# Kernel optimization log

Measured on AMD Instinct MI355X. Metric: run time of the kernel, lower is better.

The kernel has to match this reference:

```python
import jax, jax.numpy as jnp
import numpy as np

B, S, D = 4, 2048, 768
H = 12
DH = D // H  # 64
DF = 2048
THETA = 10000.0
EPS = 1e-5


def setup_inputs() -> dict:
    key = jax.random.key(0)
    ks = jax.random.split(key, 8)
    sc = 0.02  # keep activations numerically tame
    return {
        "x": jax.random.normal(ks[0], (B, S, D), jnp.float32),
        "ln1_w": jnp.ones((D,), jnp.float32),
        "ln2_w": jnp.ones((D,), jnp.float32),
        "p_q": jax.random.normal(ks[1], (D, D), jnp.float32) * sc,
        "p_k": jax.random.normal(ks[2], (D, D), jnp.float32) * sc,
        "p_v": jax.random.normal(ks[3], (D, D), jnp.float32) * sc,
        "p_o": jax.random.normal(ks[4], (D, D), jnp.float32) * sc,
        "w1": jax.random.normal(ks[5], (DF, D), jnp.float32) * sc,
        "w2": jax.random.normal(ks[6], (D, DF), jnp.float32) * sc,
        "w3": jax.random.normal(ks[7], (DF, D), jnp.float32) * sc,
    }


def _rmsnorm(x, w):
    # matches torch: fp32 compute, mean-square + eps
    rms = jnp.sqrt(jnp.mean(x * x, axis=-1, keepdims=True) + EPS)
    return x / rms * w


def _rope(t):
    # t: [B, H, S, DH]; rotation per RoPE matrix: pairs (2k, 2k+1)
    pos = jnp.arange(S, dtype=jnp.float32)[:, None]            # [S,1]
    k = jnp.arange(DH // 2, dtype=jnp.float32)[None, :]        # [1,DH/2]
    ang = pos / (THETA ** (2.0 * k / DH))                      # [S,DH/2]
    cos, sin = jnp.cos(ang), jnp.sin(ang)
    t2 = t.reshape(*t.shape[:-1], DH // 2, 2)
    x0, x1 = t2[..., 0], t2[..., 1]
    o0 = cos * x0 - sin * x1
    o1 = sin * x0 + cos * x1
    return jnp.stack([o0, o1], axis=-1).reshape(t.shape)


def reference(x, ln1_w, ln2_w, p_q, p_k, p_v, p_o, w1, w2, w3):
    # --- attention sublayer ---
    h = _rmsnorm(x, ln1_w)                                     # [B,S,D]
    Wq = p_q.reshape(H, DH, D)
    Wk = p_k.reshape(H, DH, D)
    Wv = p_v.reshape(H, DH, D)
    q = _rope(jnp.einsum('bsd,hed->bhse', h, Wq))              # [B,H,S,DH]
    k = _rope(jnp.einsum('bsd,hed->bhse', h, Wk))
    v = jnp.einsum('bsd,hed->bhse', h, Wv)
    scores = jnp.einsum('bhqe,bhke->bhqk', q, k)               # [B,H,S,S]
    mask = jnp.tril(jnp.ones((S, S), bool))
    scores = jnp.where(mask, scores, -jnp.inf)
    attn = jax.nn.softmax(scores / jnp.sqrt(jnp.float32(DH)), axis=-1)
    ctx = jnp.einsum('bhqk,bhke->bhqe', attn, v)               # [B,H,S,DH]
    ctx = jnp.transpose(ctx, (0, 2, 1, 3)).reshape(B, S, D)    # [B,S,D]
    x = x + ctx @ p_o.T
    # --- SwiGLU FFN sublayer ---
    h2 = _rmsnorm(x, ln2_w)
    u1 = h2 @ w1.T
    u1 = u1 * jax.nn.sigmoid(u1)                               # SiLU
    u3 = h2 @ w3.T
    x = x + (u1 * u3) @ w2.T
    return x
```

## Files before the change

### kernel.cpp

```cpp
#include <hip/hip_runtime.h>
#include <stdint.h>

#define B_  4
#define S_  2048
#define D_  768
#define H_  12
#define DH_ 64
#define DF_ 2048
#define M_  (B_*S_)
#define NQKV 2304
#define N13  4096

typedef __attribute__((ext_vector_type(8))) short bf16x8;
typedef __attribute__((ext_vector_type(4))) short bf16x4;
typedef __attribute__((ext_vector_type(4))) float f32x4;
typedef unsigned short u16;

#if !defined(__HIP_DEVICE_COMPILE__)
  #define MFMA_K16(A,B,C) (C)
#elif __has_builtin(__builtin_amdgcn_mfma_f32_16x16x16_bf16)
  #define MFMA_K16(A,B,C) __builtin_amdgcn_mfma_f32_16x16x16_bf16((A),(B),(C),0,0,0)
#else
  #define MFMA_K16(A,B,C) __builtin_amdgcn_mfma_f32_16x16x16bf16_1k((A),(B),(C),0,0,0)
#endif

__device__ __forceinline__ float bf2f(u16 v) {
  union { uint32_t u; float f; } x; x.u = ((uint32_t)v) << 16; return x.f;
}
__device__ __forceinline__ u16 f2bf(float f) {
  union { float f; uint32_t u; } x; x.f = f;
  uint32_t r = x.u + 0x7FFFu + ((x.u >> 16) & 1u);
  return (u16)(r >> 16);
}
__device__ __forceinline__ void gl_lds16(const u16* g, u16* l) {
  __builtin_amdgcn_global_load_lds((const __attribute__((address_space(1))) uint32_t*)g,
                                   (__attribute__((address_space(3))) uint32_t*)l, 16, 0, 0);
}

__global__ __launch_bounds__(256) void cast_all_kernel(const float* __restrict__ pq,
                                                       const float* __restrict__ pk,
                                                       const float* __restrict__ pv,
                                                       const float* __restrict__ po,
                                                       const float* __restrict__ w2,
                                                       u16* __restrict__ wqkv,
                                                       u16* __restrict__ wob,
                                                       u16* __restrict__ w2b) {
  int bidx = blockIdx.x;
  const float* src; u16* dst; int off;
  if (bidx < 576)       { src = pq; dst = wqkv;           off = bidx; }
  else if (bidx < 1152) { src = pk; dst = wqkv + 589824;  off = bidx - 576; }
  else if (bidx < 1728) { src = pv; dst = wqkv + 1179648; off = bidx - 1152; }
  else if (bidx < 2304) { src = po; dst = wob;            off = bidx - 1728; }
  else                  { src = w2; dst = w2b;            off = bidx - 2304; }
  int i = off * 256 + threadIdx.x;
  float4 v = ((const float4*)src)[i];
  ushort4 o;
  o.x = f2bf(v.x); o.y = f2bf(v.y); o.z = f2bf(v.z); o.w = f2bf(v.w);
  ((ushort4*)dst)[i] = o;
}

__global__ __launch_bounds__(192) void cast_w13_kernel(const float* __restrict__ w1,
                                                       const float* __restrict__ w3,
                                                       u16* __restrict__ out) {
  int j = blockIdx.x, which = blockIdx.y;
  const float* src = (which ? w3 : w1) + (size_t)j * D_;
  int fr = (j >> 4) * 32 + (j & 15) + which * 16;
  u16* dst = out + (size_t)fr * D_;
  int t = threadIdx.x;
  float4 v = ((const float4*)src)[t];
  ushort4 o;
  o.x = f2bf(v.x); o.y = f2bf(v.y); o.z = f2bf(v.z); o.w = f2bf(v.w);
  ((ushort4*)dst)[t] = o;
}

__global__ __launch_bounds__(256) void rmsnorm_kernel(const float* __restrict__ x,
                                                      const float* __restrict__ w,
                                                      u16* __restrict__ out) {
  int row = blockIdx.x, tid = threadIdx.x;
  const float* xr = x + (size_t)row * D_;
  float v0 = xr[tid], v1 = xr[tid + 256], v2 = xr[tid + 512];
  float ss = v0 * v0 + v1 * v1 + v2 * v2;
  #pragma unroll
  for (int m = 32; m >= 1; m >>= 1) ss += __shfl_xor(ss, m, 64);
  __shared__ float red[4];
  if ((tid & 63) == 0) red[tid >> 6] = ss;
  __syncthreads();
  float tot = red[0] + red[1] + red[2] + red[3];
  float r = rsqrtf(tot * (1.0f / D_) + 1e-5f);
  u16* o = out + (size_t)row * D_;
  o[tid]       = f2bf(v0 * r * w[tid]);
  o[tid + 256] = f2bf(v1 * r * w[tid + 256]);
  o[tid + 512] = f2bf(v2 * r * w[tid + 512]);
}

template<int MT, int EPI>
__global__ __launch_bounds__(256) void gemm_bt_kernel(const u16* __restrict__ A,
                                                      const u16* __restrict__ W,
                                                      void* __restrict__ Cout,
                                                      const float* __restrict__ res,
                                                      u16* __restrict__ vTout,
                                                      int K, int N) {
  constexpr int ABELEMS = MT * 64 + 128 * 64;
  constexpr int SMELEMS = (EPI == 3 && 128 * 132 > ABELEMS) ? 128 * 132 : ABELEMS;
  __shared__ __align__(16) u16 smem[SMELEMS];
  u16* As = smem;
  u16* Bs = smem + MT * 64;
  constexpr int MI = MT / 32;
  int tid = threadIdx.x;
  int wave = tid >> 6, lane = tid & 63;
  int quad = lane >> 4, l16 = lane & 15;
  int wr = (wave >> 1) * (MT / 2), wc = (wave & 1) * 64;
  int gx = gridDim.x;
  int lin = blockIdx.y * gx + blockIdx.x;
  int cpx = (gx * gridDim.y) >> 3;
  int nlin = (lin & 7) * cpx + (lin >> 3);
  int m0 = (nlin / gx) * MT, n0 = (nlin % gx) * 128;
  f32x4 acc[MI][4] = {};
  for (int kt = 0; kt < K; kt += 64) {
    __syncthreads();
    #pragma unroll
    for (int i = 0; i < MT / 32; ++i) {
      int idx = i * 256 + tid;
      int r = idx >> 3, c = idx & 7;
      gl_lds16(&A[(size_t)(m0 + r) * K + kt + ((c ^ (r & 7)) * 8)], &As[(i * 256 + wave * 64) * 8]);
    }
    #pragma unroll
    for (int i = 0; i < 4; ++i) {
      int idx = i * 256 + tid;
      int r = idx >> 3, c = idx & 7;
      gl_lds16(&W[(size_t)(n0 + r) * K + kt + ((c ^ (r & 7)) * 8)], &Bs[(i * 256 + wave * 64) * 8]);
    }
    __syncthreads();
    #pragma unroll
    for (int ks = 0; ks < 2; ++ks) {
      bf16x8 af[MI], bf[4];
      int sw = ((ks * 4 + quad) ^ (l16 & 7)) * 8;
      #pragma unroll
      for (int t = 0; t < MI; ++t)
        af[t] = *(const bf16x8*)&As[(wr + t * 16 + l16) * 64 + sw];
      #pragma unroll
      for (int t = 0; t < 4; ++t)
        bf[t] = *(const bf16x8*)&Bs[(wc + t * 16 + l16) * 64 + sw];
      #pragma unroll
      for (int mt = 0; mt < MI; ++mt)
        #pragma unroll
        for (int nt = 0; nt < 4; ++nt)
          acc[mt][nt] = __builtin_amdgcn_mfma_f32_16x16x32_bf16(af[mt], bf[nt], acc[mt][nt], 0, 0, 0);
    }
  }

  if (EPI == 3 && n0 >= 1536) {
    __syncthreads();
    #pragma unroll
    for (int mt = 0; mt < MI; ++mt) {
      int sloc = wr + mt * 16 + quad * 4;
      #pragma unroll
      for (int nt = 0; nt < 4; ++nt) {
        int col = wc + nt * 16 + l16;
        ushort4 o;
        o.x = f2bf(acc[mt][nt][0]); o.y = f2bf(acc[mt][nt][1]);
        o.z = f2bf(acc[mt][nt][2]); o.w = f2bf(acc[mt][nt][3]);
        *(ushort4*)&smem[col * 132 + sloc] = o;
      }
    }
    __syncthreads();
    int b = m0 >> 11, sblk = m0 & 2047;
    #pragma unroll
    for (int i = 0; i < 8; ++i) {
      int idx = i * 256 + tid;
      int row = idx >> 4, c16 = idx & 15;
      uint4 d = *(const uint4*)&smem[row * 132 + c16 * 8];
      int vg = n0 - 1536 + row;
      int h = vg >> 6, dh = vg & 63;
      *(uint4*)&vTout[((size_t)(b * H_ + h) * 64 + dh) * (size_t)S_ + sblk + c16 * 8] = d;
    }
  } else if (EPI == 3) {
    bool isq = (n0 < 768);
    float osc = isq ? 0.18033688f : 1.0f;
    #pragma unroll
    for (int mt = 0; mt < MI; ++mt) {
      int r0 = m0 + wr + mt * 16 + quad * 4;
      int pos0 = r0 & 2047;
      #pragma unroll
      for (int nt = 0; nt < 4; ++nt) {
        int col = n0 + wc + nt * 16 + l16;
        int kk = (col & 63) >> 1;
        float freq = exp2f(-0.41524101186092035f * (float)kk);
        bool odd = (col & 1);
        #pragma unroll
        for (int r = 0; r < 4; ++r) {
          float own = acc[mt][nt][r];
          float pv = __shfl_xor(own, 1, 64);
          float ang = (float)(pos0 + r) * freq;
          float sv, cv;
          __sincosf(ang, &sv, &cv);
          float o = odd ? (sv * pv + cv * own) : (cv * own - sv * pv);
          ((u16*)Cout)[(size_t)(r0 + r) * N + col] = f2bf(o * osc);
        }
      }
    }
  } else {
    #pragma unroll
    for (int mt = 0; mt < MI; ++mt) {
      #pragma unroll
      for (int r = 0; r < 4; ++r) {
        int gr = m0 + wr + mt * 16 + quad * 4 + r;
        if (EPI == 2) {
          #pragma unroll
          for (int np = 0; np < 2; ++np) {
            float u1v = acc[mt][np * 2][r], u3v = acc[mt][np * 2 + 1][r];
            float sg = 1.0f / (1.0f + __builtin_amdgcn_exp2f(-u1v * 1.44269504f));
            float g = u1v * sg * u3v;
            int gc = (n0 >> 1) + (wave & 1) * 32 + np * 16 + l16;
            ((u16*)Cout)[(size_t)gr * (N >> 1) + gc] = f2bf(g);
          }
        } else {
          #pragma unroll
          for (int nt = 0; nt < 4; ++nt) {
            int gc = n0 + wc + nt * 16 + l16;
            size_t off = (size_t)gr * N + gc;
            float vv = acc[mt][nt][r];
            if (EPI == 1) ((float*)Cout)[off] = vv + res[off];
            else          ((u16*)Cout)[off] = f2bf(vv);
          }
        }
      }
    }
  }
}

#define FENCE() asm volatile("" ::: "memory")
#define BAR() do { FENCE(); __builtin_amdgcn_s_barrier(); FENCE(); } while (0)
#define LGKM0() do { asm volatile("s_waitcnt lgkmcnt(0)" ::: "memory"); \
                     __builtin_amdgcn_sched_barrier(0); } while (0)

template<int MH, int NH>
__device__ __forceinline__ void quad_mfma(f32x4 (&acc)[2][4][2][2],
                                          const bf16x8 (&ra)[4][2],
                                          const bf16x8 (&rb)[2][2]) {
  #pragma unroll
  for (int ks = 0; ks < 2; ++ks)
    #pragma unroll
    for (int mt = 0; mt < 4; ++mt)
      #pragma unroll
      for (int nt = 0; nt < 2; ++nt)
        acc[MH][mt][NH][nt] =
          __builtin_amdgcn_mfma_f32_16x16x32_bf16(ra[mt][ks], rb[nt][ks], acc[MH][mt][NH][nt], 0, 0, 0);
}

__device__ __forceinline__ void ld_af(bf16x8 (&rr)[4][2], const u16* base,
                                      int wrow, int l16, int quad) {
  #pragma unroll
  for (int mt = 0; mt < 4; ++mt)
    #pragma unroll
    for (int ks = 0; ks < 2; ++ks)
      rr[mt][ks] = *(const bf16x8*)&base[(wrow + mt * 16 + l16) * 64 +
                                         (((ks * 4 + quad) ^ (l16 & 7)) * 8)];
}
__device__ __forceinline__ void ld_bf(bf16x8 (&rr)[2][2], const u16* base,
                                      int wrow, int l16, int quad) {
  #pragma unroll
  for (int nt = 0; nt < 2; ++nt)
    #pragma unroll
    for (int ks = 0; ks < 2; ++ks)
      rr[nt][ks] = *(const bf16x8*)&base[(wrow + nt * 16 + l16) * 64 +
                                         (((ks * 4 + quad) ^ (l16 & 7)) * 8)];
}

template<int EPI, int K, int N>
__global__ __launch_bounds__(512, 2) void gemm256_kernel(const u16* __restrict__ A,
                                                         const u16* __restrict__ W,
                                                         void* __restrict__ Cout,
                                                         const float* __restrict__ res) {
  __shared__ __align__(16) u16 smem[2][2][2][128 * 64];
  int tid = threadIdx.x;
  int wave = tid >> 6, lane = tid & 63;
  int quad = lane >> 4, l16 = lane & 15;
  int wm = wave >> 2, wn = wave & 3;
  constexpr int GX = N / 256, NB = GX * (M_ / 256), CPX = NB / 8;
  int lin = blockIdx.y * GX + blockIdx.x;
  int nlin = (lin & 7) * CPX + (lin >> 3);
  int m0 = (nlin / GX) * 256, n0 = (nlin % GX) * 256;
  constexpr int NI = (K >> 6) >> 1;

  f32x4 acc[2][4][2][2] = {};
  bf16x8 rA[4][2], rBlo[2][2], rBhi[2][2];

  int r0 = tid >> 3, c0 = tid & 7;
  int scb = (c0 ^ (r0 & 7)) * 16;
  uint32_t offA = (uint32_t)(m0 + r0) * (uint32_t)(K * 2) + (uint32_t)scb;
  uint32_t offB = (uint32_t)(n0 + r0) * (uint32_t)(K * 2) + (uint32_t)scb;

  #define STG(kof, ab, h, bufi) do {                                               \
    const char* _s = (ab) ? (const char*)W : (const char*)A;                       \
    uint32_t _o = ((ab) ? offB : offA) + (uint32_t)((kof) + (h) * (128 * K * 2));  \
    u16* _d = &smem[bufi][ab][h][wave * 512];                                      \
    gl_lds16((const u16*)(_s + _o), _d);                                           \
    gl_lds16((const u16*)(_s + _o + 64 * K * 2), _d + 4096);                       \
  } while (0)

  int wrA = wm * 64, wrB = wn * 32;

  STG(0, 0, 0, 0); STG(0, 1, 0, 0); STG(0, 1, 1, 0); STG(0, 0, 1, 0);
  STG(128, 0, 0, 1); STG(128, 1, 0, 1); STG(128, 1, 1, 1); STG(128, 0, 1, 1);
  offA += 256; offB += 256;
  asm volatile("s_waitcnt vmcnt(8)" ::: "memory");
  BAR();
  ld_af(rA,   &smem[0][0][0][0], wrA, l16, quad);
  ld_bf(rBlo, &smem[0][1][0][0], wrB, l16, quad);
  LGKM0();
  BAR();

  #define G256_ITER(MORE) do {                                                     \
                                                                     \
    ld_bf(rBhi, &smem[0][1][1][0], wrB, l16, quad);                                \
    if (MORE) STG(0, 0, 0, 0);                                                     \
    BAR(); LGKM0();                                                                \
    __builtin_amdgcn_s_setprio(1); quad_mfma<0, 0>(acc, rA, rBlo);                 \
    __builtin_amdgcn_s_setprio(0); BAR();                                          \
                                                   \
    if (MORE) STG(0, 1, 0, 0);                                                     \
    BAR(); LGKM0();                                                                \
    __builtin_amdgcn_s_setprio(1); quad_mfma<0, 1>(acc, rA, rBhi);                 \
    __builtin_amdgcn_s_setprio(0);                                                 \
    ld_af(rA, &smem[0][0][1][0], wrA, l16, quad);                                  \
    BAR();                                                                         \
                                                   \
    if (MORE) STG(0, 1, 1, 0);                                                     \
    BAR(); LGKM0();                                                                \
    __builtin_amdgcn_s_setprio(1); quad_mfma<1, 0>(acc, rA, rBlo);                 \
    __builtin_amdgcn_s_setprio(0);                                                 \
    if (MORE) asm volatile("s_waitcnt vmcnt(6)" ::: "memory");                     \
    else      asm volatile("s_waitcnt vmcnt(0)" ::: "memory");                     \
    BAR();                                                                         \
                                    \
    ld_bf(rBlo, &smem[1][1][0][0], wrB, l16, quad);                                \
    if (MORE) STG(0, 0, 1, 0);                                                     \
    BAR(); LGKM0();                                                                \
    __builtin_amdgcn_s_setprio(1); quad_mfma<1, 1>(acc, rA, rBhi);                 \
    __builtin_amdgcn_s_setprio(0);                                                 \
    ld_af(rA, &smem[1][0][0][0], wrA, l16, quad);                                  \
    BAR();                                                                         \
                                                                \
    ld_bf(rBhi, &smem[1][1][1][0], wrB, l16, quad);                                \
    if (MORE) STG(128, 0, 0, 1);                                                   \
    BAR(); LGKM0();                                                                \
    __builtin_amdgcn_s_setprio(1); quad_mfma<0, 0>(acc, rA, rBlo);                 \
    __builtin_amdgcn_s_setprio(0); BAR();                                          \
                                                   \
    if (MORE) STG(128, 1, 0, 1);                                                   \
    BAR(); LGKM0();                                                                \
    __builtin_amdgcn_s_setprio(1); quad_mfma<0, 1>(acc, rA, rBhi);                 \
    __builtin_amdgcn_s_setprio(0);                                                 \
    ld_af(rA, &smem[1][0][1][0], wrA, l16, quad);                                  \
    BAR();                                                                         \
                                                   \
    if (MORE) STG(128, 1, 1, 1);                                                   \
    BAR(); LGKM0();                                                                \
    __builtin_amdgcn_s_setprio(1); quad_mfma<1, 0>(acc, rA, rBlo);                 \
    __builtin_amdgcn_s_setprio(0);                                                 \
    if (MORE) asm volatile("s_waitcnt vmcnt(6)" ::: "memory");                     \
    else      asm volatile("s_waitcnt vmcnt(0)" ::: "memory");                     \
    BAR();                                                                         \
                                    \
    if (MORE) ld_bf(rBlo, &smem[0][1][0][0], wrB, l16, quad);                      \
    if (MORE) STG(128, 0, 1, 1);                                                   \
    BAR(); LGKM0();                                                                \
    __builtin_amdgcn_s_setprio(1); quad_mfma<1, 1>(acc, rA, rBhi);                 \
    __builtin_amdgcn_s_setprio(0);                                                 \
    if (MORE) ld_af(rA, &smem[0][0][0][0], wrA, l16, quad);                        \
    BAR();                                                                         \
  } while (0)

  #pragma unroll 1
  for (int i = 0; i < NI - 1; ++i) {
    G256_ITER(true);
    offA += 256; offB += 256;
  }
  G256_ITER(false);
  #undef G256_ITER
  #undef STG

  if (EPI == 2) {
    const int Nh = N >> 1;
    #pragma unroll
    for (int mh = 0; mh < 2; ++mh)
      #pragma unroll
      for (int mt = 0; mt < 4; ++mt)
        #pragma unroll
        for (int r = 0; r < 4; ++r) {
          int gr = m0 + mh * 128 + wm * 64 + mt * 16 + quad * 4 + r;
          #pragma unroll
          for (int nh = 0; nh < 2; ++nh) {
            float u1v = acc[mh][mt][nh][0][r], u3v = acc[mh][mt][nh][1][r];
            float sg = 1.0f / (1.0f + __builtin_amdgcn_exp2f(-u1v * 1.44269504f));
            float g = u1v * sg * u3v;
            int gc = (n0 >> 1) + nh * 64 + wn * 16 + l16;
            ((u16*)Cout)[(size_t)gr * Nh + gc] = f2bf(g);
          }
        }
  } else if (EPI == 1) {
    #pragma unroll
    for (int mh = 0; mh < 2; ++mh)
      #pragma unroll
      for (int mt = 0; mt < 4; ++mt)
        #pragma unroll
        for (int r = 0; r < 4; ++r) {
          int gr = m0 + mh * 128 + wm * 64 + mt * 16 + quad * 4 + r;
          #pragma unroll
          for (int nh = 0; nh < 2; ++nh)
            #pragma unroll
            for (int nt = 0; nt < 2; ++nt) {
              int gc = n0 + nh * 128 + wn * 32 + nt * 16 + l16;
              size_t off = (size_t)gr * N + gc;
              ((float*)Cout)[off] = acc[mh][mt][nh][nt][r] + res[off];
            }
        }
  } else {
    #pragma unroll
    for (int mh = 0; mh < 2; ++mh)
      #pragma unroll
      for (int mt = 0; mt < 4; ++mt)
        #pragma unroll
        for (int r = 0; r < 4; ++r) {
          int gr = m0 + mh * 128 + wm * 64 + mt * 16 + quad * 4 + r;
          #pragma unroll
          for (int nh = 0; nh < 2; ++nh)
            #pragma unroll
            for (int nt = 0; nt < 2; ++nt) {
              int gc = n0 + nh * 128 + wn * 32 + nt * 16 + l16;
              ((u16*)Cout)[(size_t)gr * N + gc] = f2bf(acc[mh][mt][nh][nt][r]);
            }
        }
  }
}

__global__ __launch_bounds__(512, 4) void attn_kernel(const u16* __restrict__ qkv,
                                                      const u16* __restrict__ vT,
                                                      u16* __restrict__ ctx) {
  __shared__ __align__(16) u16 Ks[128 * 64];
  __shared__ __align__(16) u16 Vt[64 * 128];
  int bh = blockIdx.x;
  int qt = 15 - blockIdx.y;
  int b = bh / H_, h = bh % H_;
  const u16* qbase = qkv + (size_t)b * S_ * NQKV + h * DH_;
  const u16* kbase = qbase + 768;
  const u16* vtb   = vT + (size_t)bh * 64 * S_;
  int tid = threadIdx.x, wave = tid >> 6, lane = tid & 63;
  int quad = lane >> 4, l16 = lane & 15;
  const float MFIX = 12.0f;

  bf16x8 qf[2];
  int qrow = qt * 128 + wave * 16 + l16;
  qf[0] = *(const bf16x8*)&qbase[(size_t)qrow * NQKV + quad * 8];
  qf[1] = *(const bf16x8*)&qbase[(size_t)qrow * NQKV + 32 + quad * 8];
  f32x4 oacc[4] = {};
  float lsum = 0.f;
  int nkt = qt + 1;
  for (int kt = 0; kt < nkt; ++kt) {
    __syncthreads();
    #pragma unroll
    for (int i = 0; i < 2; ++i) {
      int idx = i * 512 + tid;
      int r = idx >> 3, c = idx & 7;
      gl_lds16(&kbase[(size_t)(kt * 128 + r) * NQKV + ((c ^ (r & 7)) * 8)],
               &Ks[(i * 512 + wave * 64) * 8]);
    }
    #pragma unroll
    for (int i = 0; i < 2; ++i) {
      int idx = i * 512 + tid;
      int d = idx >> 4, c16 = idx & 15;
      gl_lds16(&vtb[(size_t)d * S_ + kt * 128 + ((c16 ^ (d & 15)) * 8)],
               &Vt[(i * 512 + wave * 64) * 8]);
    }
    __syncthreads();
    bool diag = (kt == nkt - 1);
    #pragma unroll
    for (int t = 0; t < 8; ++t) {
      if (diag && t > wave) break;
      f32x4 sc = {};
      #pragma unroll
      for (int c = 0; c < 2; ++c) {
        bf16x8 kf = *(const bf16x8*)&Ks[(t * 16 + l16) * 64 + (((c * 4 + quad) ^ (l16 & 7)) * 8)];
        sc = __builtin_amdgcn_mfma_f32_16x16x32_bf16(kf, qf[c], sc, 0, 0, 0);
      }
      float p[4];
      #pragma unroll
      for (int r = 0; r < 4; ++r) p[r] = __builtin_amdgcn_exp2f(sc[r] - MFIX);
      if (diag && t == wave) {
        #pragma unroll
        for (int r = 0; r < 4; ++r)
          if (quad * 4 + r > l16) p[r] = 0.f;
      }
      lsum += (p[0] + p[1]) + (p[2] + p[3]);
      uint32_t lo = ((__float_as_uint(p[0]) + 0x8000u) >> 16) |
                    ((__float_as_uint(p[1]) + 0x8000u) & 0xFFFF0000u);
      uint32_t hi = ((__float_as_uint(p[2]) + 0x8000u) >> 16) |
                    ((__float_as_uint(p[3]) + 0x8000u) & 0xFFFF0000u);
      uint2 pk; pk.x = lo; pk.y = hi;
      bf16x4 pf = *(bf16x4*)&pk;
      #pragma unroll
      for (int n = 0; n < 4; ++n) {
        bf16x4 vf = *(const bf16x4*)&Vt[(n * 16 + l16) * 128 +
                                        (((t * 2 + (quad >> 1)) ^ l16) * 8) + (quad & 1) * 4];
        oacc[n] = MFMA_K16(vf, pf, oacc[n]);
      }
    }
  }
  float l = lsum;
  l += __shfl_xor(l, 16, 64);
  l += __shfl_xor(l, 32, 64);
  float inv = 1.0f / l;
  #pragma unroll
  for (int n = 0; n < 4; ++n) {
    ushort4 o;
    o.x = f2bf(oacc[n][0] * inv);
    o.y = f2bf(oacc[n][1] * inv);
    o.z = f2bf(oacc[n][2] * inv);
    o.w = f2bf(oacc[n][3] * inv);
    *(ushort4*)&ctx[(size_t)(b * S_ + qrow) * D_ + h * DH_ + n * 16 + quad * 4] = o;
  }
}

#define WQKV_OFF 0u
#define W13_OFF  3538944u
#define W2_OFF   9830400u
#define WO_OFF   12976128u
#define HB_OFF   14155776u
#define QKV_OFF  26738688u
#define VT_OFF   64487424u
#define X1_OFF   77070336u
#define G_OFF    102236160u

extern "C" void kernel_launch(void* const* d_in, const int* in_sizes, int n_in,
                              void* d_out, int out_size, void* d_ws, size_t ws_size,
                              hipStream_t stream) {
  const float* x    = (const float*)d_in[0];
  const float* ln1w = (const float*)d_in[1];
  const float* ln2w = (const float*)d_in[2];
  const float* pq   = (const float*)d_in[3];
  const float* pk   = (const float*)d_in[4];
  const float* pv   = (const float*)d_in[5];
  const float* po   = (const float*)d_in[6];
  const float* w1   = (const float*)d_in[7];
  const float* w2   = (const float*)d_in[8];
  const float* w3   = (const float*)d_in[9];
  char* ws = (char*)d_ws;
  u16* wqkv = (u16*)(ws + WQKV_OFF);
  u16* w13b = (u16*)(ws + W13_OFF);
  u16* w2b  = (u16*)(ws + W2_OFF);
  u16* wob  = (u16*)(ws + WO_OFF);
  u16* hb   = (u16*)(ws + HB_OFF);
  u16* qkvb = (u16*)(ws + QKV_OFF);
  u16* vtb  = (u16*)(ws + VT_OFF);
  u16* cb   = (u16*)(ws + HB_OFF);
  float* x1 = (float*)(ws + X1_OFF);
  u16* h2b  = (u16*)(ws + VT_OFF);
  u16* gb   = (u16*)(ws + G_OFF);

  cast_all_kernel<<<3840, 256, 0, stream>>>(pq, pk, pv, po, w2, wqkv, wob, w2b);
  cast_w13_kernel<<<dim3(2048, 2), 192, 0, stream>>>(w1, w3, w13b);

  rmsnorm_kernel<<<M_, 256, 0, stream>>>(x, ln1w, hb);
  gemm_bt_kernel<128, 3><<<dim3(18, 64), 256, 0, stream>>>(hb, wqkv, qkvb, nullptr, vtb, 768, NQKV);
  attn_kernel<<<dim3(48, 16), 512, 0, stream>>>(qkvb, vtb, cb);
  gemm_bt_kernel<64, 1><<<dim3(6, 128), 256, 0, stream>>>(cb, wob, x1, x, nullptr, 768, 768);

  rmsnorm_kernel<<<M_, 256, 0, stream>>>(x1, ln2w, h2b);
  gemm256_kernel<2, 768, N13><<<dim3(N13 / 256, M_ / 256), 512, 0, stream>>>(h2b, w13b, gb, nullptr);
  gemm_bt_kernel<64, 1><<<dim3(6, 128), 256, 0, stream>>>(gb, w2b, (float*)d_out, x1, nullptr, 2048, 768);
}
```

Measured before the change: 329.9 us.

## Move QKV projection to 256x256 pipelined GEMM with RoPE and V-transpose epilogue

Runs the QKV projection through the larger 256x256 tile, 512-thread, double-buffered GEMM kernel instead of the 128x128 generic one. The RoPE/scale epilogue and the shared-memory V transpose are ported to that kernel's accumulator layout, and the old epilogues are removed from the generic kernel. Larger tiles raise data reuse and MFMA efficiency, but with N=2304 the grid is only 9x32 = 288 blocks, which may fill the GPU poorly. The transpose now needs two staged passes through shared memory.

Result: no change. 323.5 us, median of 2 (-1.9%).

```diff
diff --git a/kernel.cpp b/kernel.cpp
--- a/kernel.cpp
+++ b/kernel.cpp
@@ -101,8 +101,7 @@
                                                       u16* __restrict__ vTout,
                                                       int K, int N) {
   constexpr int ABELEMS = MT * 64 + 128 * 64;
-  constexpr int SMELEMS = (EPI == 3 && 128 * 132 > ABELEMS) ? 128 * 132 : ABELEMS;
-  __shared__ __align__(16) u16 smem[SMELEMS];
+  __shared__ __align__(16) u16 smem[ABELEMS];
   u16* As = smem;
   u16* Bs = smem + MT * 64;
   constexpr int MI = MT / 32;
@@ -149,81 +148,18 @@
     }
   }
 
-  if (EPI == 3 && n0 >= 1536) {
-    __syncthreads();
-    #pragma unroll
-    for (int mt = 0; mt < MI; ++mt) {
-      int sloc = wr + mt * 16 + quad * 4;
+  #pragma unroll
+  for (int mt = 0; mt < MI; ++mt) {
+    #pragma unroll
+    for (int r = 0; r < 4; ++r) {
+      int gr = m0 + wr + mt * 16 + quad * 4 + r;
       #pragma unroll
       for (int nt = 0; nt < 4; ++nt) {
-        int col = wc + nt * 16 + l16;
-        ushort4 o;
-        o.x = f2bf(acc[mt][nt][0]); o.y = f2bf(acc[mt][nt][1]);
-        o.z = f2bf(acc[mt][nt][2]); o.w = f2bf(acc[mt][nt][3]);
-        *(ushort4*)&smem[col * 132 + sloc] = o;
-      }
-    }
-    __syncthreads();
-    int b = m0 >> 11, sblk = m0 & 2047;
-    #pragma unroll
-    for (int i = 0; i < 8; ++i) {
-      int idx = i * 256 + tid;
-      int row = idx >> 4, c16 = idx & 15;
-      uint4 d = *(const uint4*)&smem[row * 132 + c16 * 8];
-      int vg = n0 - 1536 + row;
-      int h = vg >> 6, dh = vg & 63;
-      *(uint4*)&vTout[((size_t)(b * H_ + h) * 64 + dh) * (size_t)S_ + sblk + c16 * 8] = d;
-    }
-  } else if (EPI == 3) {
-    bool isq = (n0 < 768);
-    float osc = isq ? 0.18033688f : 1.0f;
-    #pragma unroll
-    for (int mt = 0; mt < MI; ++mt) {
-      int r0 = m0 + wr + mt * 16 + quad * 4;
-      int pos0 = r0 & 2047;
-      #pragma unroll
-      for (int nt = 0; nt < 4; ++nt) {
-        int col = n0 + wc + nt * 16 + l16;
-        int kk = (col & 63) >> 1;
-        float freq = exp2f(-0.41524101186092035f * (float)kk);
-        bool odd = (col & 1);
-        #pragma unroll
-        for (int r = 0; r < 4; ++r) {
-          float own = acc[mt][nt][r];
-          float pv = __shfl_xor(own, 1, 64);
-          float ang = (float)(pos0 + r) * freq;
-          float sv, cv;
-          __sincosf(ang, &sv, &cv);
-          float o = odd ? (sv * pv + cv * own) : (cv * own - sv * pv);
-          ((u16*)Cout)[(size_t)(r0 + r) * N + col] = f2bf(o * osc);
-        }
-      }
-    }
-  } else {
-    #pragma unroll
-    for (int mt = 0; mt < MI; ++mt) {
-      #pragma unroll
-      for (int r = 0; r < 4; ++r) {
-        int gr = m0 + wr + mt * 16 + quad * 4 + r;
-        if (EPI == 2) {
-          #pragma unroll
-          for (int np = 0; np < 2; ++np) {
-            float u1v = acc[mt][np * 2][r], u3v = acc[mt][np * 2 + 1][r];
-            float sg = 1.0f / (1.0f + __builtin_amdgcn_exp2f(-u1v * 1.44269504f));
-            float g = u1v * sg * u3v;
-            int gc = (n0 >> 1) + (wave & 1) * 32 + np * 16 + l16;
-            ((u16*)Cout)[(size_t)gr * (N >> 1) + gc] = f2bf(g);
-          }
-        } else {
-          #pragma unroll
-          for (int nt = 0; nt < 4; ++nt) {
-            int gc = n0 + wc + nt * 16 + l16;
-            size_t off = (size_t)gr * N + gc;
-            float vv = acc[mt][nt][r];
-            if (EPI == 1) ((float*)Cout)[off] = vv + res[off];
-            else          ((u16*)Cout)[off] = f2bf(vv);
-          }
-        }
+        int gc = n0 + wc + nt * 16 + l16;
+        size_t off = (size_t)gr * N + gc;
+        float vv = acc[mt][nt][r];
+        if (EPI == 1) ((float*)Cout)[off] = vv + res[off];
+        else          ((u16*)Cout)[off] = f2bf(vv);
       }
     }
   }
@@ -271,7 +207,8 @@
 __global__ __launch_bounds__(512, 2) void gemm256_kernel(const u16* __restrict__ A,
                                                          const u16* __restrict__ W,
                                                          void* __restrict__ Cout,
-                                                         const float* __restrict__ res) {
+                                                         const float* __restrict__ res,
+                                                         u16* __restrict__ vTout) {
   __shared__ __align__(16) u16 smem[2][2][2][128 * 64];
   int tid = threadIdx.x;
   int wave = tid >> 6, lane = tid & 63;
@@ -381,7 +318,73 @@
   #undef G256_ITER
   #undef STG
 
-  if (EPI == 2) {
+  if (EPI == 3) {
+    if (n0 >= 1536) {
+      u16* sm = &smem[0][0][0][0];
+      int b = m0 >> 11, sblk = m0 & 2047;
+      #pragma unroll
+      for (int mh = 0; mh < 2; ++mh) {
+        BAR();
+        #pragma unroll
+        for (int mt = 0; mt < 4; ++mt) {
+          int rl4 = wm * 64 + mt * 16 + quad * 4;
+          #pragma unroll
+          for (int nh = 0; nh < 2; ++nh)
+            #pragma unroll
+            for (int nt = 0; nt < 2; ++nt) {
+              int cl = nh * 128 + wn * 32 + nt * 16 + l16;
+              ushort4 o;
+              o.x = f2bf(acc[mh][mt][nh][nt][0]);
+              o.y = f2bf(acc[mh][mt][nh][nt][1]);
+              o.z = f2bf(acc[mh][mt][nh][nt][2]);
+              o.w = f2bf(acc[mh][mt][nh][nt][3]);
+              *(ushort4*)&sm[cl * 132 + rl4] = o;
+            }
+        }
+        BAR();
+        #pragma unroll
+        for (int i = 0; i < 8; ++i) {
+          int idx = i * 512 + tid;
+          int cl = idx >> 4, c16 = idx & 15;
+          uint4 d = *(const uint4*)&sm[cl * 132 + c16 * 8];
+          int vg = n0 - 1536 + cl;
+          int h = vg >> 6, dh = vg & 63;
+          *(uint4*)&vTout[((size_t)(b * H_ + h) * 64 + dh) * (size_t)S_ +
+                          sblk + mh * 128 + c16 * 8] = d;
+        }
+      }
+    } else {
+      bool isq = (n0 < 768);
+      float osc = isq ? 0.18033688f : 1.0f;
+      bool odd = (l16 & 1);
+      #pragma unroll
+      for (int nt = 0; nt < 2; ++nt) {
+        int kk = (((wn & 1) * 32 + nt * 16 + l16) & 63) >> 1;
+        float freq = exp2f(-0.41524101186092035f * (float)kk);
+        #pragma unroll
+        for (int mh = 0; mh < 2; ++mh)
+          #pragma unroll
+          for (int mt = 0; mt < 4; ++mt) {
+            int gr0 = m0 + mh * 128 + wm * 64 + mt * 16 + quad * 4;
+            int pos0 = gr0 & 2047;
+            #pragma unroll
+            for (int r = 0; r < 4; ++r) {
+              float ang = (float)(pos0 + r) * freq;
+              float sv, cv;
+              __sincosf(ang, &sv, &cv);
+              #pragma unroll
+              for (int nh = 0; nh < 2; ++nh) {
+                float own = acc[mh][mt][nh][nt][r];
+                float pv = __shfl_xor(own, 1, 64);
+                float o = odd ? (sv * pv + cv * own) : (cv * own - sv * pv);
+                ((u16*)Cout)[(size_t)(gr0 + r) * N +
+                             n0 + nh * 128 + wn * 32 + nt * 16 + l16] = f2bf(o * osc);
+              }
+            }
+          }
+      }
+    }
+  } else if (EPI == 2) {
     const int Nh = N >> 1;
     #pragma unroll
     for (int mh = 0; mh < 2; ++mh)
@@ -562,11 +565,11 @@
   cast_w13_kernel<<<dim3(2048, 2), 192, 0, stream>>>(w1, w3, w13b);
 
   rmsnorm_kernel<<<M_, 256, 0, stream>>>(x, ln1w, hb);
-  gemm_bt_kernel<128, 3><<<dim3(18, 64), 256, 0, stream>>>(hb, wqkv, qkvb, nullptr, vtb, 768, NQKV);
+  gemm256_kernel<3, 768, NQKV><<<dim3(NQKV / 256, M_ / 256), 512, 0, stream>>>(hb, wqkv, qkvb, nullptr, vtb);
   attn_kernel<<<dim3(48, 16), 512, 0, stream>>>(qkvb, vtb, cb);
   gemm_bt_kernel<64, 1><<<dim3(6, 128), 256, 0, stream>>>(cb, wob, x1, x, nullptr, 768, 768);
 
   rmsnorm_kernel<<<M_, 256, 0, stream>>>(x1, ln2w, h2b);
-  gemm256_kernel<2, 768, N13><<<dim3(N13 / 256, M_ / 256), 512, 0, stream>>>(h2b, w13b, gb, nullptr);
+  gemm256_kernel<2, 768, N13><<<dim3(N13 / 256, M_ / 256), 512, 0, stream>>>(h2b, w13b, gb, nullptr, nullptr);
   gemm_bt_kernel<64, 1><<<dim3(6, 128), 256, 0, stream>>>(gb, w2b, (float*)d_out, x1, nullptr, 2048, 768);
 }
```
